# Optimization experiments

Measured on AMD Instinct MI355X. Metric: run time of the kernel, lower is better.

## Reference

```python
import jax, jax.numpy as jnp
import numpy as np

L, N, E, D, H = 3, 20000, 320000, 128, 4
EPS = 1.1920929e-07  # torch RMSNorm default eps = finfo(float32).eps
NEG_SLOPE = 0.2      # PyG GATConv leaky_relu negative_slope


def rmsnorm(x, w):
    return x * jax.lax.rsqrt(jnp.mean(x * x, axis=-1, keepdims=True) + EPS) * w


def setup_inputs() -> dict:
    key = jax.random.key(0)
    ks = jax.random.split(key, 13)
    s = 0.02
    x = jax.random.normal(ks[0], (N, D), jnp.float32)
    src = jax.random.randint(ks[1], (E,), 0, N, dtype=jnp.int64)
    dst = jax.random.randint(ks[2], (E,), 0, N, dtype=jnp.int64)
    dst = jnp.where(dst == src, (dst + 1) % N, dst)  # no pre-existing self loops
    edge_index = jnp.stack([src, dst])
    return {
        "x": x,
        "W_gat": jax.random.normal(ks[3], (L, D, H * D), jnp.float32) * s,
        "att_src": jax.random.normal(ks[4], (L, H, D), jnp.float32) * s,
        "att_dst": jax.random.normal(ks[5], (L, H, D), jnp.float32) * s,
        "bias_gat": jax.random.normal(ks[6], (L, D), jnp.float32) * s,
        "W1": jax.random.normal(ks[7], (L, D, D), jnp.float32) * s,
        "b1": jax.random.normal(ks[8], (L, D), jnp.float32) * s,
        "W2": jax.random.normal(ks[9], (L, D, D), jnp.float32) * s,
        "b2": jax.random.normal(ks[10], (L, D), jnp.float32) * s,
        "norm1_w": jnp.ones((L, D), jnp.float32),
        "norm2_w": jnp.ones((L, D), jnp.float32),
        "edge_index": edge_index,
    }


def reference(x, W_gat, att_src, att_dst, bias_gat, W1, b1, W2, b2, norm1_w, norm2_w, edge_index):
    # PyG GATConv adds self loops by default
    loops = jnp.arange(N, dtype=edge_index.dtype)
    src = jnp.concatenate([edge_index[0], loops])  # [E+N]
    dst = jnp.concatenate([edge_index[1], loops])
    for i in range(L):
        # --- GATConv(hidden, hidden, heads=H, concat=False), dropout=0 (eval) ---
        xp = (x @ W_gat[i]).reshape(N, H, D)               # [N,H,D]
        a_s = jnp.einsum('nhd,hd->nh', xp, att_src[i])     # [N,H]
        a_d = jnp.einsum('nhd,hd->nh', xp, att_dst[i])
        e = jax.nn.leaky_relu(a_s[src] + a_d[dst], NEG_SLOPE)  # [E+N,H]
        m = jax.ops.segment_max(e, dst, num_segments=N)
        ex = jnp.exp(e - m[dst])
        denom = jax.ops.segment_sum(ex, dst, num_segments=N)
        alpha = ex / denom[dst]                             # segment softmax over incoming edges
        agg = jax.ops.segment_sum(alpha[:, :, None] * xp[src], dst, num_segments=N)  # [N,H,D]
        x_att = agg.mean(axis=1) + bias_gat[i]              # concat=False -> head mean, then bias
        # --- residual + RMSNorm ---
        x = rmsnorm(x + x_att, norm1_w[i])
        # --- FFN ---
        h = jax.nn.relu(x @ W1[i] + b1[i])
        h = h @ W2[i] + b2[i]
        x = rmsnorm(x + h, norm2_w[i])
    return x
```

## Files before the change

kernel.cpp:

```cpp
#include <hip/hip_runtime.h>
#include <hip/hip_bf16.h>

#define N_NODES 20000
#define NEDGE   320000
#define DIM     128
#define NH      4
#define HD      512
#define LAYERS  3
#define EPS_RMS 1.1920929e-07f
#define SLOPE   0.2f
#define NTILES  (N_NODES >> 4)

#define NWGC  (LAYERS * DIM * HD)
#define NW1C  (LAYERS * DIM * DIM)
#define NVC   (LAYERS * DIM)
#define NPACK (NWGC + 2 * NW1C + 5 * NVC)
#define NXV   (N_NODES * DIM / 8)

typedef __bf16 bf16_t;
typedef __bf16 bf16v2 __attribute__((ext_vector_type(2)));
typedef __bf16 bf16v8 __attribute__((ext_vector_type(8)));
typedef float  f32v4  __attribute__((ext_vector_type(4)));
typedef float  f32v2  __attribute__((ext_vector_type(2)));

__device__ __forceinline__ int clamp_node(int s) {
    return ((unsigned)s >= (unsigned)N_NODES) ? 0 : s;
}
__device__ __forceinline__ float leaky(float e) { return e > 0.f ? e : SLOPE * e; }
__device__ __forceinline__ unsigned char enc_fp8(float v) {
    int p = __builtin_amdgcn_cvt_pk_fp8_f32(v, v, 0, false);
    return (unsigned char)(p & 0xff);
}
__device__ __forceinline__ unsigned short enc_fp8_pair(float a, float b) {
    int p = __builtin_amdgcn_cvt_pk_fp8_f32(a, b, 0, false);
    return (unsigned short)(p & 0xffff);
}

__device__ __forceinline__ bool wave_detect_bf16(const unsigned short* xh) {
    int lane = threadIdx.x & 63;
    unsigned short hw = xh[2 * lane];
    int e = (hw >> 7) & 0xff;
    unsigned long long b = __ballot(e >= 96 && e <= 140);
    return __popcll(b) >= 48;
}
__device__ __forceinline__ bool wave_detect_i64(const int* ei) {
    int lane = threadIdx.x & 63;
    unsigned long long b = __ballot(ei[2 * lane + 1] != 0);
    return b == 0ULL;
}
__device__ __forceinline__ float raw_elem(const void* in, size_t j, bool isbf) {
    return isbf ? (float)((const bf16_t*)in)[j] : ((const float*)in)[j];
}
__device__ __forceinline__ bf16_t cvt_elem(const void* in, size_t j, bool isbf) {
    return isbf ? ((const bf16_t*)in)[j] : (bf16_t)((const float*)in)[j];
}
__device__ __forceinline__ int edge_src(const int* ei, int e, bool is64) {
    return clamp_node(is64 ? ei[2 * e] : ei[e]);
}
__device__ __forceinline__ int edge_dst(const int* ei, int e, bool is64) {
    return clamp_node(is64 ? ei[2 * NEDGE + 2 * e] : ei[NEDGE + e]);
}

__global__ __launch_bounds__(256) void prep_v(const void* x, const void* Wg,
                                              const void* aS, const void* aD,
                                              float* __restrict__ vS, float* __restrict__ vD,
                                              int* __restrict__ deg) {
    int gid = blockIdx.x * 256 + threadIdx.x;
    for (int i = gid; i < N_NODES; i += gridDim.x * 256) deg[i] = 0;
    bool isbf = wave_detect_bf16((const unsigned short*)x);
    int w = gid >> 6;
    if (w >= LAYERS * DIM * NH * 2) return;
    int lane = threadIdx.x & 63;
    int sd = w & 1, h = (w >> 1) & 3, k = (w >> 3) & 127, l = w >> 10;
    const void* att = sd ? aD : aS;
    size_t wbase = (size_t)l * DIM * HD + (size_t)k * HD + h * DIM;
    size_t abase = (size_t)l * NH * DIM + (size_t)h * DIM;
    int c = 2 * lane;
    float p = raw_elem(Wg, wbase + c, isbf) * raw_elem(att, abase + c, isbf)
            + raw_elem(Wg, wbase + c + 1, isbf) * raw_elem(att, abase + c + 1, isbf);
#pragma unroll
    for (int msk = 1; msk < 64; msk <<= 1) p += __shfl_xor(p, msk);
    if (lane == 0) {
        float* dst = sd ? vD : vS;
        dst[l * HD + h * DIM + k] = p;
    }
}

__device__ __forceinline__ void pack_item(int i, bool isbf,
        const void* Wg, const void* W1, const void* W2,
        const void* bg, const void* b1, const void* b2,
        const void* n1, const void* n2,
        bf16_t* WmixP, bf16_t* W1P, bf16_t* W2P,
        bf16_t* bgc, bf16_t* b1c, bf16_t* b2c, bf16_t* n1c, bf16_t* n2c) {
    if (i < NWGC) {
        int l = i >> 16;
        int r = i & 65535;
        int j = r & 7;
        int lane2 = (r >> 3) & 63;
        int mm = lane2 & 15, kqq = lane2 >> 4;
        int tt = (r >> 9) & 1;
        int kk = (r >> 10) & 15;
        int wvv = r >> 14;
        int kidx = kk * 32 + kqq * 8 + j;
        int h = kidx >> 7, kp = kidx & 127;
        int c = 32 * wvv + tt * 16 + mm;
        WmixP[i] = cvt_elem(Wg, (size_t)l * DIM * HD + (size_t)kp * HD + h * DIM + c, isbf);
        return;
    }
    i -= NWGC;
    if (i < NW1C) {
        int l = i / 16384;
        int r = i & 16383;
        int j = r & 7;
        int lane2 = (r >> 3) & 63;
        int mm = lane2 & 15, kqq = lane2 >> 4;
        int tt = (r >> 9) & 1;
        int ks = (r >> 10) & 3;
        int wvv = r >> 12;
        int k = ks * 32 + kqq * 8 + j;
        int c = 32 * wvv + tt * 16 + mm;
        W1P[i] = cvt_elem(W1, (size_t)l * DIM * DIM + (size_t)k * DIM + c, isbf);
        return;
    }
    i -= NW1C;
    if (i < NW1C) {
        int l = i / 16384;
        int r = i & 16383;
        int j = r & 7;
        int lane2 = (r >> 3) & 63;
        int mm = lane2 & 15, kqq = lane2 >> 4;
        int tt = (r >> 9) & 1;
        int ks = (r >> 10) & 3;
        int wvv = r >> 12;
        int k = ks * 32 + kqq * 8 + j;
        int c = 32 * wvv + tt * 16 + mm;
        W2P[i] = cvt_elem(W2, (size_t)l * DIM * DIM + (size_t)k * DIM + c, isbf);
        return;
    }
    i -= NW1C;
    if (i >= 5 * NVC) return;
    int seg = i / NVC, k = i - seg * NVC;
    if (seg == 0) bgc[k] = cvt_elem(bg, k, isbf);
    else if (seg == 1) b1c[k] = cvt_elem(b1, k, isbf);
    else if (seg == 2) b2c[k] = cvt_elem(b2, k, isbf);
    else if (seg == 3) n1c[k] = cvt_elem(n1, k, isbf);
    else n2c[k] = cvt_elem(n2, k, isbf);
}

__global__ __launch_bounds__(256) void mega_setup(
        const void* x, const void* Wg, const void* W1, const void* W2,
        const void* bg, const void* b1, const void* b2, const void* n1, const void* n2,
        bf16_t* xb, bf16_t* WmixP, bf16_t* W1P, bf16_t* W2P,
        bf16_t* bgc, bf16_t* b1c, bf16_t* b2c, bf16_t* n1c, bf16_t* n2c,
        const int* ei, int* deg,
        const float* vS, const float* vD,
        float* a_s, float* a_d, unsigned short* x8,
        int convBlocks, int histBlocks) {
    int b = (int)blockIdx.x;
    if (b >= convBlocks + histBlocks) {
        bool isbf = wave_detect_bf16((const unsigned short*)x);
        int lane = threadIdx.x & 63;
        int n = (b - convBlocks - histBlocks) * 4 + (int)(threadIdx.x >> 6);
        if (n >= N_NODES) return;
        int c = 2 * lane;
        float f0 = raw_elem(x, (size_t)n * DIM + c, isbf);
        float f1 = raw_elem(x, (size_t)n * DIM + c + 1, isbf);
        x8[n * 64 + lane] = enc_fp8_pair(f0, f1);
#pragma unroll
        for (int h = 0; h < NH; ++h) {
            float ps = f0 * vS[h * DIM + c] + f1 * vS[h * DIM + c + 1];
            float pd = f0 * vD[h * DIM + c] + f1 * vD[h * DIM + c + 1];
#pragma unroll
            for (int msk = 1; msk < 64; msk <<= 1) {
                ps += __shfl_xor(ps, msk);
                pd += __shfl_xor(pd, msk);
            }
            if (lane == 0) {
                a_s[n * 4 + h] = ps;
                a_d[n * 4 + h] = pd;
            }
        }
        return;
    }
    if (b >= convBlocks) {
        bool is64 = wave_detect_i64(ei);
        int e = (b - convBlocks) * 256 + threadIdx.x;
        if (e < NEDGE) atomicAdd(&deg[edge_dst(ei, e, is64)], 1);
        return;
    }
    bool isbf = wave_detect_bf16((const unsigned short*)x);
    int i = b * 256 + threadIdx.x;
    if (i < NXV) {
        if (isbf) {
            ((bf16v8*)xb)[i] = ((const bf16v8*)x)[i];
        } else {
            const float4* src = (const float4*)x;
            float4 a = src[2 * i], bq = src[2 * i + 1];
            bf16v8 o;
            o[0] = (bf16_t)a.x;  o[1] = (bf16_t)a.y;
            o[2] = (bf16_t)a.z;  o[3] = (bf16_t)a.w;
            o[4] = (bf16_t)bq.x; o[5] = (bf16_t)bq.y;
            o[6] = (bf16_t)bq.z; o[7] = (bf16_t)bq.w;
            ((bf16v8*)xb)[i] = o;
        }
        return;
    }
    pack_item(i - NXV, isbf, Wg, W1, W2, bg, b1, b2, n1, n2,
              WmixP, W1P, W2P, bgc, b1c, b2c, n1c, n2c);
}

__global__ __launch_bounds__(1024) void scan_kernel(const int* __restrict__ deg,
                                                    int* __restrict__ row_ptr,
                                                    int* __restrict__ cursor) {
    __shared__ int wsum[16];
    int tid = threadIdx.x, lane = tid & 63, wv = tid >> 6;
    int v[20];
    int base = tid * 20;
    int tot = 0;
    if (base < N_NODES) {
        const int4* d4 = reinterpret_cast<const int4*>(deg + base);
#pragma unroll
        for (int j = 0; j < 5; ++j) {
            int4 q = d4[j];
            v[4 * j]     = q.x;
            v[4 * j + 1] = q.y;
            v[4 * j + 2] = q.z;
            v[4 * j + 3] = q.w;
        }
#pragma unroll
        for (int i = 0; i < 20; ++i) tot += v[i];
    }
    int x = tot;
#pragma unroll
    for (int off = 1; off < 64; off <<= 1) {
        int t = __shfl_up(x, off);
        if (lane >= off) x += t;
    }
    if (lane == 63) wsum[wv] = x;
    __syncthreads();
    if (wv == 0) {
        int s = (lane < 16) ? wsum[lane] : 0;
#pragma unroll
        for (int off = 1; off < 16; off <<= 1) {
            int t = __shfl_up(s, off);
            if (lane >= off) s += t;
        }
        if (lane < 16) wsum[lane] = s;
    }
    __syncthreads();
    int off0 = ((wv == 0) ? 0 : wsum[wv - 1]) + (x - tot);
    if (tid == 0) row_ptr[0] = 0;
    if (base < N_NODES) {
        int run = off0;
#pragma unroll
        for (int i = 0; i < 20; ++i) {
            run += v[i];
            row_ptr[base + i + 1] = run;
            cursor[base + i] = run - v[i];
        }
    }
}

__global__ void fill_kernel(const int* __restrict__ ei, int* __restrict__ cursor,
                            int* __restrict__ csr_src) {
    bool is64 = wave_detect_i64(ei);
    int e = blockIdx.x * blockDim.x + threadIdx.x;
    if (e < NEDGE) {
        int d = edge_dst(ei, e, is64);
        int pos = atomicAdd(&cursor[d], 1);
        if ((unsigned)pos < (unsigned)NEDGE) csr_src[pos] = edge_src(ei, e, is64);
    }
}

__device__ __forceinline__ void acc8(float (&acc)[8], const float4 w, unsigned short xe) {
    f32v2 f = __builtin_amdgcn_cvt_pk_f32_fp8((int)xe, false);
    acc[0] += w.x * f[0]; acc[1] += w.x * f[1];
    acc[2] += w.y * f[0]; acc[3] += w.y * f[1];
    acc[4] += w.z * f[0]; acc[5] += w.z * f[1];
    acc[6] += w.w * f[0]; acc[7] += w.w * f[1];
}

__device__ __forceinline__ void acc_group_loop(float (&acc)[8], int cnt,
        const float4* wshw, const int* sshw,
        const unsigned short* __restrict__ x8, int lane) {
    unsigned short xA[8], xB[8];
    {
        int pa = cnt < 8 ? cnt : 8;
        int pb = cnt - 8; if (pb > 8) pb = 8;
#pragma unroll
        for (int u = 0; u < 8; ++u)
            if (u < pa) xA[u] = x8[sshw[u] + lane];
#pragma unroll
        for (int u = 0; u < 8; ++u)
            if (u < pb) xB[u] = x8[sshw[8 + u] + lane];
    }
    for (int u0 = 0; u0 < cnt; u0 += 16) {
        {
            unsigned short xc[8];
#pragma unroll
            for (int u = 0; u < 8; ++u) xc[u] = xA[u];
            int g = u0 + 16;
            int nc = cnt - g; if (nc > 8) nc = 8;
#pragma unroll
            for (int u = 0; u < 8; ++u)
                if (u < nc) xA[u] = x8[sshw[g + u] + lane];
            int uc = cnt - u0; if (uc > 8) uc = 8;
#pragma unroll
            for (int u = 0; u < 8; ++u)
                if (u < uc) acc8(acc, wshw[u0 + u], xc[u]);
        }
        if (u0 + 8 < cnt) {
            unsigned short xc[8];
#pragma unroll
            for (int u = 0; u < 8; ++u) xc[u] = xB[u];
            int g = u0 + 24;
            int nc = cnt - g; if (nc > 8) nc = 8;
#pragma unroll
            for (int u = 0; u < 8; ++u)
                if (u < nc) xB[u] = x8[sshw[g + u] + lane];
            int uc = cnt - (u0 + 8); if (uc > 8) uc = 8;
#pragma unroll
            for (int u = 0; u < 8; ++u)
                if (u < uc) acc8(acc, wshw[u0 + 8 + u], xc[u]);
        }
    }
}

__device__ __forceinline__ void gat_phaseA(int tile, int lane, const int rw[4],
        float4* wshw, int* sshw,
        const int* __restrict__ row_ptr, const int* __restrict__ csr_src,
        const float* __restrict__ a_s, const float* __restrict__ a_d,
        const unsigned short* __restrict__ x8, bf16_t (*ylds)[524]) {
    const float4* a_s4 = reinterpret_cast<const float4*>(a_s);
    const float4* a_d4 = reinterpret_cast<const float4*>(a_d);

    int beg[4], deg[4];
#pragma unroll
    for (int rp = 0; rp < 4; ++rp) {
        int nn = tile * 16 + rw[rp];
        int b = row_ptr[nn], e = row_ptr[nn + 1];
        int d = e - b;
        if (d < 0) d = 0;
        if (d > NEDGE) d = NEDGE;
        if (b < 0) b = 0;
        if (b > NEDGE - d) b = NEDGE - d;
        beg[rp] = b; deg[rp] = d;
    }

    int craw[4], sreg[4];
    unsigned short pslf[4];
    float4 av4[4], adv4[4], avs4[4];

    {
        int d = deg[0];
        int idx = (d > 0) ? (beg[0] + (lane < d ? lane : 0)) : 0;
        craw[0] = csr_src[idx];
        d = deg[1];
        idx = (d > 0) ? (beg[1] + (lane < d ? lane : 0)) : 0;
        craw[1] = csr_src[idx];
        int nn = tile * 16 + rw[0];
        adv4[0] = a_d4[nn];
        avs4[0] = a_s4[nn];
        pslf[0] = x8[nn * 64 + lane];
        int s = clamp_node(craw[0]);
        sreg[0] = s;
        av4[0] = a_s4[s];
    }

#pragma unroll
    for (int rp = 0; rp < 4; ++rp) {
        float4 adv = adv4[rp];
        float4 a0 = av4[rp];
        float4 wl = {__expf(leaky(a0.x + adv.x)), __expf(leaky(a0.y + adv.y)),
                     __expf(leaky(a0.z + adv.z)), __expf(leaky(a0.w + adv.w))};
        float4 avs = avs4[rp];
        float4 wself = {__expf(leaky(avs.x + adv.x)), __expf(leaky(avs.y + adv.y)),
                        __expf(leaky(avs.z + adv.z)), __expf(leaky(avs.w + adv.w))};
        float acc[8];
        {
            f32v2 f = __builtin_amdgcn_cvt_pk_f32_fp8((int)pslf[rp], false);
            acc[0] = wself.x * f[0]; acc[1] = wself.x * f[1];
            acc[2] = wself.y * f[0]; acc[3] = wself.y * f[1];
            acc[4] = wself.z * f[0]; acc[5] = wself.z * f[1];
            acc[6] = wself.w * f[0]; acc[7] = wself.w * f[1];
        }
        int cnt0 = deg[rp] < 64 ? deg[rp] : 64;
        float4 zl = {0.f, 0.f, 0.f, 0.f};
        if (lane < cnt0) {
            zl = wl;
            wshw[lane] = wl;
            sshw[lane] = sreg[rp] << 6;
        }

        if (rp < 3) {
            int nn = tile * 16 + rw[rp + 1];
            adv4[rp + 1] = a_d4[nn];
            avs4[rp + 1] = a_s4[nn];
            pslf[rp + 1] = x8[nn * 64 + lane];
            int s = clamp_node(craw[rp + 1]);
            sreg[rp + 1] = s;
            av4[rp + 1] = a_s4[s];
        }
        if (rp < 2) {
            int d = deg[rp + 2];
            int idx = (d > 0) ? (beg[rp + 2] + (lane < d ? lane : 0)) : 0;
            craw[rp + 2] = csr_src[idx];
        }

        acc_group_loop(acc, cnt0, wshw, sshw, x8, lane);

        for (int c0 = 64; c0 < deg[rp]; c0 += 64) {
            int cnt = deg[rp] - c0; if (cnt > 64) cnt = 64;
            if (lane < cnt) {
                int s = clamp_node(csr_src[beg[rp] + c0 + lane]);
                float4 a2 = a_s4[s];
                float4 w2 = {__expf(leaky(a2.x + adv.x)), __expf(leaky(a2.y + adv.y)),
                             __expf(leaky(a2.z + adv.z)), __expf(leaky(a2.w + adv.w))};
                zl.x += w2.x; zl.y += w2.y; zl.z += w2.z; zl.w += w2.w;
                wshw[lane] = w2;
                sshw[lane] = s << 6;
            }
            acc_group_loop(acc, cnt, wshw, sshw, x8, lane);
        }

        float4 zr = zl;
#pragma unroll
        for (int msk = 1; msk < 64; msk <<= 1) {
            zr.x += __shfl_xor(zr.x, msk);
            zr.y += __shfl_xor(zr.y, msk);
            zr.z += __shfl_xor(zr.z, msk);
            zr.w += __shfl_xor(zr.w, msk);
        }
        float4 z4 = {wself.x + zr.x, wself.y + zr.y, wself.z + zr.z, wself.w + zr.w};
        float4 ih4 = {1.f / z4.x, 1.f / z4.y, 1.f / z4.z, 1.f / z4.w};
        int c = 2 * lane;
        bf16_t* yrow = &ylds[rw[rp]][0];
#pragma unroll
        for (int h = 0; h < NH; ++h) {
            float ih = h == 0 ? ih4.x : h == 1 ? ih4.y : h == 2 ? ih4.z : ih4.w;
            bf16v2 o;
            o[0] = (bf16_t)(acc[h * 2 + 0] * ih);
            o[1] = (bf16_t)(acc[h * 2 + 1] * ih);
            *reinterpret_cast<bf16v2*>(&yrow[h * DIM + c]) = o;
        }
    }
}

template <int MODE>
__global__ __launch_bounds__(256) void gat_mix(
        const int* __restrict__ row_ptr, const int* __restrict__ csr_src,
        const float* __restrict__ a_s, const float* __restrict__ a_d,
        const unsigned short* __restrict__ x8,
        const bf16_t* __restrict__ WmixP, const bf16_t* __restrict__ bg,
        const bf16_t* __restrict__ n1w, const bf16_t* __restrict__ xb,
        const bf16_t* __restrict__ W1P, const bf16_t* __restrict__ b1,
        const bf16_t* __restrict__ W2P, const bf16_t* __restrict__ b2,
        const bf16_t* __restrict__ n2w, void* __restrict__ out,
        const float* __restrict__ vS, const float* __restrict__ vD,
        float* __restrict__ a_s_n, float* __restrict__ a_d_n,
        unsigned char* __restrict__ x8_n) {
    __shared__ bf16_t ylds[16][524];
    __shared__ bf16_t xm[16][140];
    __shared__ float  ssq_p[16][4];
    __shared__ float  asd_p[4][16][8];
    __shared__ float4 wsh[4][64];
    __shared__ int    ssh[4][64];
    bf16_t (*hh)[140] = reinterpret_cast<bf16_t (*)[140]>(&ylds[0][0]);

    int tile = blockIdx.x;
    int wv = threadIdx.x >> 6;
    int lane = threadIdx.x & 63;
    int m = lane & 15, kq = lane >> 4;

    int rw[4];
    {
        int d = 0;
        if (lane < 16) {
            int nn = tile * 16 + lane;
            d = row_ptr[nn + 1] - row_ptr[nn];
        }
        int rank = 0;
#pragma unroll
        for (int j = 0; j < 16; ++j) {
            int dj = __shfl(d, j);
            rank += ((dj > d) || (dj == d && j < lane)) ? 1 : 0;
        }
        if (lane >= 16) rank = 64;
        int tgt0 = wv, tgt1 = 7 - wv, tgt2 = 8 + wv, tgt3 = 15 - wv;
        rw[0] = __ffsll(__ballot(rank == tgt0)) - 1;
        rw[1] = __ffsll(__ballot(rank == tgt1)) - 1;
        rw[2] = __ffsll(__ballot(rank == tgt2)) - 1;
        rw[3] = __ffsll(__ballot(rank == tgt3)) - 1;
    }

    gat_phaseA(tile, lane, rw, wsh[wv], ssh[wv], row_ptr, csr_src, a_s, a_d, x8, ylds);
    __syncthreads();

    f32v4 accm[2];
    accm[0] = (f32v4){0.f, 0.f, 0.f, 0.f};
    accm[1] = (f32v4){0.f, 0.f, 0.f, 0.f};
#pragma unroll
    for (int kk = 0; kk < 16; ++kk) {
        bf16v8 a = *reinterpret_cast<const bf16v8*>(&ylds[m][kk * 32 + kq * 8]);
#pragma unroll
        for (int tt = 0; tt < 2; ++tt) {
            bf16v8 b = *reinterpret_cast<const bf16v8*>(
                WmixP + ((((wv * 16 + kk) * 2 + tt) << 9) + lane * 8));
            accm[tt] = __builtin_amdgcn_mfma_f32_16x16x32_bf16(a, b, accm[tt], 0, 0, 0);
        }
    }
    float vals[2][4];
    {
        float sp[4] = {0.f, 0.f, 0.f, 0.f};
#pragma unroll
        for (int tt = 0; tt < 2; ++tt) {
            int col = 32 * wv + tt * 16 + m;
            float bv = (float)bg[col];
#pragma unroll
            for (int r = 0; r < 4; ++r) {
                int gr = tile * 16 + kq * 4 + r;
                float v = 0.25f * accm[tt][r] + bv + (float)xb[(size_t)gr * DIM + col];
                vals[tt][r] = v;
                sp[r] += v * v;
            }
        }
#pragma unroll
        for (int r = 0; r < 4; ++r) {
            sp[r] += __shfl_xor(sp[r], 1); sp[r] += __shfl_xor(sp[r], 2);
            sp[r] += __shfl_xor(sp[r], 4); sp[r] += __shfl_xor(sp[r], 8);
            if (m == r) ssq_p[kq * 4 + r][wv] = sp[r];
        }
    }
    __syncthreads();
    {
#pragma unroll
        for (int r = 0; r < 4; ++r) {
            int row = kq * 4 + r;
            float s = ssq_p[row][0] + ssq_p[row][1] + ssq_p[row][2] + ssq_p[row][3];
            float scale = rsqrtf(s * (1.f / 128.f) + EPS_RMS);
#pragma unroll
            for (int tt = 0; tt < 2; ++tt) {
                int col = 32 * wv + tt * 16 + m;
                xm[row][col] = (bf16_t)(vals[tt][r] * scale * (float)n1w[col]);
            }
        }
    }
    __syncthreads();

    f32v4 acc1[2];
    acc1[0] = (f32v4){0.f, 0.f, 0.f, 0.f};
    acc1[1] = (f32v4){0.f, 0.f, 0.f, 0.f};
#pragma unroll
    for (int ks = 0; ks < 4; ++ks) {
        bf16v8 a = *reinterpret_cast<const bf16v8*>(&xm[m][ks * 32 + kq * 8]);
#pragma unroll
        for (int tt = 0; tt < 2; ++tt) {
            bf16v8 b = *reinterpret_cast<const bf16v8*>(
                W1P + ((((wv * 4 + ks) * 2 + tt) << 9) + lane * 8));
            acc1[tt] = __builtin_amdgcn_mfma_f32_16x16x32_bf16(a, b, acc1[tt], 0, 0, 0);
        }
    }
#pragma unroll
    for (int tt = 0; tt < 2; ++tt) {
        int col = 32 * wv + tt * 16 + m;
        float bv = (float)b1[col];
#pragma unroll
        for (int r = 0; r < 4; ++r) {
            float v = acc1[tt][r] + bv;
            hh[kq * 4 + r][col] = (bf16_t)(v > 0.f ? v : 0.f);
        }
    }
    __syncthreads();
    f32v4 acc2[2];
    acc2[0] = (f32v4){0.f, 0.f, 0.f, 0.f};
    acc2[1] = (f32v4){0.f, 0.f, 0.f, 0.f};
#pragma unroll
    for (int ks = 0; ks < 4; ++ks) {
        bf16v8 a = *reinterpret_cast<const bf16v8*>(&hh[m][ks * 32 + kq * 8]);
#pragma unroll
        for (int tt = 0; tt < 2; ++tt) {
            bf16v8 b = *reinterpret_cast<const bf16v8*>(
                W2P + ((((wv * 4 + ks) * 2 + tt) << 9) + lane * 8));
            acc2[tt] = __builtin_amdgcn_mfma_f32_16x16x32_bf16(a, b, acc2[tt], 0, 0, 0);
        }
    }
    float vals2[2][4];
    {
        float sp[4] = {0.f, 0.f, 0.f, 0.f};
#pragma unroll
        for (int tt = 0; tt < 2; ++tt) {
            int col = 32 * wv + tt * 16 + m;
            float bv = (float)b2[col];
#pragma unroll
            for (int r = 0; r < 4; ++r) {
                float v = acc2[tt][r] + bv + (float)xm[kq * 4 + r][col];
                vals2[tt][r] = v;
                sp[r] += v * v;
            }
        }
#pragma unroll
        for (int r = 0; r < 4; ++r) {
            sp[r] += __shfl_xor(sp[r], 1); sp[r] += __shfl_xor(sp[r], 2);
            sp[r] += __shfl_xor(sp[r], 4); sp[r] += __shfl_xor(sp[r], 8);
            if (m == r) ssq_p[kq * 4 + r][wv] = sp[r];
        }
    }
    __syncthreads();
    float o2[2][4];
#pragma unroll
    for (int r = 0; r < 4; ++r) {
        int row = kq * 4 + r;
        int gr = tile * 16 + row;
        float s = ssq_p[row][0] + ssq_p[row][1] + ssq_p[row][2] + ssq_p[row][3];
        float scale = rsqrtf(s * (1.f / 128.f) + EPS_RMS);
#pragma unroll
        for (int tt = 0; tt < 2; ++tt) {
            int col = 32 * wv + tt * 16 + m;
            float o = vals2[tt][r] * scale * (float)n2w[col];
            o2[tt][r] = o;
            if (MODE == 1) ((float*)out)[(size_t)gr * DIM + col] = o;
            else {
                ((bf16_t*)out)[(size_t)gr * DIM + col] = (bf16_t)o;
                x8_n[(size_t)gr * DIM + col] = enc_fp8(o);
            }
        }
    }
    if (MODE == 0) {
        float vs0[NH], vs1[NH], vd0[NH], vd1[NH];
        int col0 = 32 * wv + m, col1 = col0 + 16;
#pragma unroll
        for (int h = 0; h < NH; ++h) {
            vs0[h] = vS[h * DIM + col0]; vs1[h] = vS[h * DIM + col1];
            vd0[h] = vD[h * DIM + col0]; vd1[h] = vD[h * DIM + col1];
        }
#pragma unroll
        for (int r = 0; r < 4; ++r) {
#pragma unroll
            for (int h = 0; h < NH; ++h) {
                float ps = o2[0][r] * vs0[h] + o2[1][r] * vs1[h];
                float pd = o2[0][r] * vd0[h] + o2[1][r] * vd1[h];
                ps += __shfl_xor(ps, 1); ps += __shfl_xor(ps, 2);
                ps += __shfl_xor(ps, 4); ps += __shfl_xor(ps, 8);
                pd += __shfl_xor(pd, 1); pd += __shfl_xor(pd, 2);
                pd += __shfl_xor(pd, 4); pd += __shfl_xor(pd, 8);
                if (m == r * 4 + h) {
                    asd_p[wv][kq * 4 + r][h * 2 + 0] = ps;
                    asd_p[wv][kq * 4 + r][h * 2 + 1] = pd;
                }
            }
        }
        __syncthreads();
        int t = threadIdx.x;
        if (t < 128) {
            int row = t >> 3, idx = t & 7;
            float s = asd_p[0][row][idx] + asd_p[1][row][idx]
                    + asd_p[2][row][idx] + asd_p[3][row][idx];
            int gr = tile * 16 + row;
            if (idx & 1) a_d_n[gr * 4 + (idx >> 1)] = s;
            else         a_s_n[gr * 4 + (idx >> 1)] = s;
        }
    }
}

extern "C" void kernel_launch(void* const* d_in, const int* in_sizes, int n_in,
                              void* d_out, int out_size, void* d_ws, size_t ws_size,
                              hipStream_t stream) {
    const void* x_in   = d_in[0];
    const void* W_gat  = d_in[1];
    const void* att_s  = d_in[2];
    const void* att_d  = d_in[3];
    const void* bias_g = d_in[4];
    const void* W1     = d_in[5];
    const void* b1     = d_in[6];
    const void* W2     = d_in[7];
    const void* b2     = d_in[8];
    const void* n1w    = d_in[9];
    const void* n2w    = d_in[10];
    const int*  ei     = (const int*)d_in[11];

    char* ws = (char*)d_ws;
    size_t off = 0;
    auto alloc = [&](size_t bytes) {
        void* p = ws + off;
        off = (off + bytes + 255) & ~(size_t)255;
        return p;
    };
    bf16_t* WmixP   = (bf16_t*)alloc((size_t)LAYERS * HD * DIM * 2);
    bf16_t* W1P     = (bf16_t*)alloc((size_t)LAYERS * DIM * DIM * 2);
    bf16_t* W2P     = (bf16_t*)alloc((size_t)LAYERS * DIM * DIM * 2);
    bf16_t* xb      = (bf16_t*)alloc((size_t)N_NODES * DIM * 2);
    unsigned short* x8a = (unsigned short*)alloc((size_t)N_NODES * DIM);
    unsigned short* x8b = (unsigned short*)alloc((size_t)N_NODES * DIM);
    float*  vS      = (float*)alloc((size_t)LAYERS * HD * 4);
    float*  vD      = (float*)alloc((size_t)LAYERS * HD * 4);
    float*  a_sA    = (float*)alloc((size_t)N_NODES * NH * 4);
    float*  a_dA    = (float*)alloc((size_t)N_NODES * NH * 4);
    float*  a_sB    = (float*)alloc((size_t)N_NODES * NH * 4);
    float*  a_dB    = (float*)alloc((size_t)N_NODES * NH * 4);
    int*    deg     = (int*)alloc((size_t)N_NODES * 4);
    int*    cursor  = (int*)alloc((size_t)N_NODES * 4);
    int*    row_ptr = (int*)alloc((size_t)(N_NODES + 1) * 4);
    int*    csr     = (int*)alloc((size_t)NEDGE * 4);
    bf16_t* bgc     = (bf16_t*)alloc((size_t)LAYERS * DIM * 2);
    bf16_t* b1c     = (bf16_t*)alloc((size_t)LAYERS * DIM * 2);
    bf16_t* b2c     = (bf16_t*)alloc((size_t)LAYERS * DIM * 2);
    bf16_t* n1c     = (bf16_t*)alloc((size_t)LAYERS * DIM * 2);
    bf16_t* n2c     = (bf16_t*)alloc((size_t)LAYERS * DIM * 2);

    prep_v<<<(LAYERS * DIM * NH * 2 * 64 + 255) / 256, 256, 0, stream>>>(
        x_in, W_gat, att_s, att_d, vS, vD, deg);

    const int NTOT = NXV + NPACK;
    const int convBlocks = (NTOT + 255) / 256;
    const int histBlocks = (NEDGE + 255) / 256;
    const int asdBlocks  = (N_NODES + 3) / 4;
    mega_setup<<<convBlocks + histBlocks + asdBlocks, 256, 0, stream>>>(
        x_in, W_gat, W1, W2, bias_g, b1, b2, n1w, n2w,
        xb, WmixP, W1P, W2P, bgc, b1c, b2c, n1c, n2c,
        ei, deg, vS, vD, a_sA, a_dA, x8a, convBlocks, histBlocks);

    scan_kernel<<<1, 1024, 0, stream>>>(deg, row_ptr, cursor);
    fill_kernel<<<(NEDGE + 255) / 256, 256, 0, stream>>>(ei, cursor, csr);

    unsigned short* x8cur[2] = {x8a, x8b};
    float* asCur[2] = {a_sA, a_sB};
    float* adCur[2] = {a_dA, a_dB};
    for (int l = 0; l < LAYERS; ++l) {
        int ci = l & 1, ni = (l + 1) & 1;
        if (l < LAYERS - 1) {
            gat_mix<0><<<NTILES, 256, 0, stream>>>(
                row_ptr, csr, asCur[ci], adCur[ci], x8cur[ci],
                WmixP + (size_t)l * HD * DIM, bgc + (size_t)l * DIM,
                n1c + (size_t)l * DIM, xb,
                W1P + (size_t)l * DIM * DIM, b1c + (size_t)l * DIM,
                W2P + (size_t)l * DIM * DIM, b2c + (size_t)l * DIM,
                n2c + (size_t)l * DIM, xb,
                vS + (size_t)(l + 1) * HD, vD + (size_t)(l + 1) * HD,
                asCur[ni], adCur[ni], (unsigned char*)x8cur[ni]);
        } else {
            gat_mix<1><<<NTILES, 256, 0, stream>>>(
                row_ptr, csr, asCur[ci], adCur[ci], x8cur[ci],
                WmixP + (size_t)l * HD * DIM, bgc + (size_t)l * DIM,
                n1c + (size_t)l * DIM, xb,
                W1P + (size_t)l * DIM * DIM, b1c + (size_t)l * DIM,
                W2P + (size_t)l * DIM * DIM, b2c + (size_t)l * DIM,
                n2c + (size_t)l * DIM, d_out,
                nullptr, nullptr, nullptr, nullptr, nullptr);
        }
    }
}
```

Measured before the change: 278.0 us.

## Vectorize weight packing to 8-element reads and hoist all per-row gather loads

Weight packing in the setup kernel now has each thread read 8 contiguous source elements with vector loads and scatter them to the MFMA-friendly packed layout, instead of one scalar read per output element. This cuts the thread count and the number of uncoalesced global reads. In the GAT aggregation kernel, all four rows' CSR source indices and per-node a_d/a_s/self-feature loads are issued up front rather than software-pipelined one or two rows ahead. This exposes more memory-level parallelism at the cost of more live registers.

```diff
diff --git a/kernel.cpp b/kernel.cpp
--- a/kernel.cpp
+++ b/kernel.cpp
@@ -11,11 +11,11 @@
 #define SLOPE   0.2f
 #define NTILES  (N_NODES >> 4)
 
-#define NWGC  (LAYERS * DIM * HD)
-#define NW1C  (LAYERS * DIM * DIM)
 #define NVC   (LAYERS * DIM)
-#define NPACK (NWGC + 2 * NW1C + 5 * NVC)
 #define NXV   (N_NODES * DIM / 8)
+#define NWG8  (LAYERS * 512 * 16)
+#define NW18  (LAYERS * 128 * 16)
+#define NPACK8 (NWG8 + 2 * NW18 + 5 * NVC)
 
 typedef __bf16 bf16_t;
 typedef __bf16 bf16v2 __attribute__((ext_vector_type(2)));
@@ -86,60 +86,63 @@
     }
 }
 
-__device__ __forceinline__ void pack_item(int i, bool isbf,
+__device__ __forceinline__ void read8(const void* src, size_t off, bool isbf, bf16_t (&v)[8]) {
+    if (isbf) {
+        bf16v8 a = *reinterpret_cast<const bf16v8*>((const bf16_t*)src + off);
+#pragma unroll
+        for (int n = 0; n < 8; ++n) v[n] = a[n];
+    } else {
+        float4 a = *reinterpret_cast<const float4*>((const float*)src + off);
+        float4 b = *reinterpret_cast<const float4*>((const float*)src + off + 4);
+        v[0] = (bf16_t)a.x; v[1] = (bf16_t)a.y; v[2] = (bf16_t)a.z; v[3] = (bf16_t)a.w;
+        v[4] = (bf16_t)b.x; v[5] = (bf16_t)b.y; v[6] = (bf16_t)b.z; v[7] = (bf16_t)b.w;
+    }
+}
+
+__device__ __forceinline__ void pack8(int t, bool isbf,
         const void* Wg, const void* W1, const void* W2,
         const void* bg, const void* b1, const void* b2,
         const void* n1, const void* n2,
         bf16_t* WmixP, bf16_t* W1P, bf16_t* W2P,
         bf16_t* bgc, bf16_t* b1c, bf16_t* b2c, bf16_t* n1c, bf16_t* n2c) {
-    if (i < NWGC) {
-        int l = i >> 16;
-        int r = i & 65535;
-        int j = r & 7;
-        int lane2 = (r >> 3) & 63;
-        int mm = lane2 & 15, kqq = lane2 >> 4;
-        int tt = (r >> 9) & 1;
-        int kk = (r >> 10) & 15;
-        int wvv = r >> 14;
-        int kidx = kk * 32 + kqq * 8 + j;
+    if (t < NWG8) {
+        int l = t >> 13;
+        int r = t & 8191;
+        int kidx = r >> 4;
+        int c0 = (r & 15) * 8;
         int h = kidx >> 7, kp = kidx & 127;
-        int c = 32 * wvv + tt * 16 + mm;
-        WmixP[i] = cvt_elem(Wg, (size_t)l * DIM * HD + (size_t)kp * HD + h * DIM + c, isbf);
+        int kk = kidx >> 5, kqq = (kidx >> 3) & 3, j = kidx & 7;
+        int wvv = c0 >> 5, tt = (c0 >> 4) & 1, mm0 = c0 & 15;
+        size_t src = (size_t)l * DIM * HD + (size_t)kp * HD + h * DIM + c0;
+        int base = (l << 16) + (((wvv * 16 + kk) * 2 + tt) << 9) + (kqq * 16 + mm0) * 8 + j;
+        bf16_t v[8];
+        read8(Wg, src, isbf, v);
+#pragma unroll
+        for (int n = 0; n < 8; ++n) WmixP[base + n * 8] = v[n];
         return;
     }
-    i -= NWGC;
-    if (i < NW1C) {
-        int l = i / 16384;
-        int r = i & 16383;
-        int j = r & 7;
-        int lane2 = (r >> 3) & 63;
-        int mm = lane2 & 15, kqq = lane2 >> 4;
-        int tt = (r >> 9) & 1;
-        int ks = (r >> 10) & 3;
-        int wvv = r >> 12;
-        int k = ks * 32 + kqq * 8 + j;
-        int c = 32 * wvv + tt * 16 + mm;
-        W1P[i] = cvt_elem(W1, (size_t)l * DIM * DIM + (size_t)k * DIM + c, isbf);
+    t -= NWG8;
+    if (t < 2 * NW18) {
+        const void* Wsrc = (t < NW18) ? W1 : W2;
+        bf16_t* Wdst = (t < NW18) ? W1P : W2P;
+        if (t >= NW18) t -= NW18;
+        int l = t >> 11;
+        int r = t & 2047;
+        int k = r >> 4;
+        int c0 = (r & 15) * 8;
+        int ks = k >> 5, kqq = (k >> 3) & 3, j = k & 7;
+        int wvv = c0 >> 5, tt = (c0 >> 4) & 1, mm0 = c0 & 15;
+        size_t src = (size_t)l * DIM * DIM + (size_t)k * DIM + c0;
+        int base = (l << 14) + (((wvv * 4 + ks) * 2 + tt) << 9) + (kqq * 16 + mm0) * 8 + j;
+        bf16_t v[8];
+        read8(Wsrc, src, isbf, v);
+#pragma unroll
+        for (int n = 0; n < 8; ++n) Wdst[base + n * 8] = v[n];
         return;
     }
-    i -= NW1C;
-    if (i < NW1C) {
-        int l = i / 16384;
-        int r = i & 16383;
-        int j = r & 7;
-        int lane2 = (r >> 3) & 63;
-        int mm = lane2 & 15, kqq = lane2 >> 4;
-        int tt = (r >> 9) & 1;
-        int ks = (r >> 10) & 3;
-        int wvv = r >> 12;
-        int k = ks * 32 + kqq * 8 + j;
-        int c = 32 * wvv + tt * 16 + mm;
-        W2P[i] = cvt_elem(W2, (size_t)l * DIM * DIM + (size_t)k * DIM + c, isbf);
-        return;
-    }
-    i -= NW1C;
-    if (i >= 5 * NVC) return;
-    int seg = i / NVC, k = i - seg * NVC;
+    t -= 2 * NW18;
+    if (t >= 5 * NVC) return;
+    int seg = t / NVC, k = t - seg * NVC;
     if (seg == 0) bgc[k] = cvt_elem(bg, k, isbf);
     else if (seg == 1) b1c[k] = cvt_elem(b1, k, isbf);
     else if (seg == 2) b2c[k] = cvt_elem(b2, k, isbf);
@@ -205,8 +208,8 @@
         }
         return;
     }
-    pack_item(i - NXV, isbf, Wg, W1, W2, bg, b1, b2, n1, n2,
-              WmixP, W1P, W2P, bgc, b1c, b2c, n1c, n2c);
+    pack8(i - NXV, isbf, Wg, W1, W2, bg, b1, b2, n1, n2,
+          WmixP, W1P, W2P, bgc, b1c, b2c, n1c, n2c);
 }
 
 __global__ __launch_bounds__(1024) void scan_kernel(const int* __restrict__ deg,
@@ -351,17 +354,20 @@
     unsigned short pslf[4];
     float4 av4[4], adv4[4], avs4[4];
 
+#pragma unroll
+    for (int rp = 0; rp < 4; ++rp) {
+        int d = deg[rp];
+        int idx = (d > 0) ? (beg[rp] + (lane < d ? lane : 0)) : 0;
+        craw[rp] = csr_src[idx];
+    }
+#pragma unroll
+    for (int rp = 0; rp < 4; ++rp) {
+        int nn = tile * 16 + rw[rp];
+        adv4[rp] = a_d4[nn];
+        avs4[rp] = a_s4[nn];
+        pslf[rp] = x8[nn * 64 + lane];
+    }
     {
-        int d = deg[0];
-        int idx = (d > 0) ? (beg[0] + (lane < d ? lane : 0)) : 0;
-        craw[0] = csr_src[idx];
-        d = deg[1];
-        idx = (d > 0) ? (beg[1] + (lane < d ? lane : 0)) : 0;
-        craw[1] = csr_src[idx];
-        int nn = tile * 16 + rw[0];
-        adv4[0] = a_d4[nn];
-        avs4[0] = a_s4[nn];
-        pslf[0] = x8[nn * 64 + lane];
         int s = clamp_node(craw[0]);
         sreg[0] = s;
         av4[0] = a_s4[s];
@@ -393,18 +399,9 @@
         }
 
         if (rp < 3) {
-            int nn = tile * 16 + rw[rp + 1];
-            adv4[rp + 1] = a_d4[nn];
-            avs4[rp + 1] = a_s4[nn];
-            pslf[rp + 1] = x8[nn * 64 + lane];
             int s = clamp_node(craw[rp + 1]);
             sreg[rp + 1] = s;
             av4[rp + 1] = a_s4[s];
-        }
-        if (rp < 2) {
-            int d = deg[rp + 2];
-            int idx = (d > 0) ? (beg[rp + 2] + (lane < d ? lane : 0)) : 0;
-            craw[rp + 2] = csr_src[idx];
         }
 
         acc_group_loop(acc, cnt0, wshw, sshw, x8, lane);
@@ -710,7 +707,7 @@
     prep_v<<<(LAYERS * DIM * NH * 2 * 64 + 255) / 256, 256, 0, stream>>>(
         x_in, W_gat, att_s, att_d, vS, vD, deg);
 
-    const int NTOT = NXV + NPACK;
+    const int NTOT = NXV + NPACK8;
     const int convBlocks = (NTOT + 255) / 256;
     const int histBlocks = (NEDGE + 255) / 256;
     const int asdBlocks  = (N_NODES + 3) / 4;
```

After: 276.6 us. About the same (-0.5%).
